# Kernel optimization log

Hardware: AMD Instinct MI355X
Metric: run time of the kernel (lower is better)

## Reference

```python
import jax, jax.numpy as jnp
import numpy as np

R = 8  # number_of_remaining_feature_maps
NEG_SLOPE = 0.01  # torch LeakyReLU default


def setup_inputs() -> dict:
    key = jax.random.key(0)
    k0, k1, k2, k3, k4 = jax.random.split(key, 5)
    b, c, D, H, W = 8, 64, 48, 48, 48
    x = jax.random.normal(k0, (b, c, D, H, W), dtype=jnp.float32)
    s = 1.0 / np.sqrt(c)
    w1 = jax.random.uniform(k1, (c, c), jnp.float32, -s, s)
    b1 = jax.random.uniform(k2, (c,), jnp.float32, -s, s)
    w2 = jax.random.uniform(k3, (c, c), jnp.float32, -s, s)
    b2 = jax.random.uniform(k4, (c,), jnp.float32, -s, s)
    return {"x": x, "w1": w1, "b1": b1, "w2": w2, "b2": b2}


def reference(x, w1, b1, w2, b2):
    # x: (b, c, D, H, W)
    y = jnp.mean(x, axis=(2, 3, 4))                       # adaptive avg pool -> (b, c)
    y = jax.nn.leaky_relu(y @ w1.T + b1, NEG_SLOPE)       # Linear + LeakyReLU
    y = jax.nn.sigmoid(y @ w2.T + b2)                     # Linear + Sigmoid
    _, idx = jax.lax.top_k(y, R)                          # (b, R) channel indices
    # batched channel gather: (b, R, D, H, W)
    return jnp.take_along_axis(x, idx[:, :, None, None, None], axis=1)
```

## Files before the change

### kernel.cpp

```cpp
#include <hip/hip_runtime.h>
#include <math.h>

#define NCH 64
#define NB 8
#define RSEL 8
#define SPATIAL 110592
#define S4 27648
#define PARTS 4
#define CHUNK4 (S4 / PARTS)
#define ITERS (CHUNK4 / 256)

__global__ __launch_bounds__(256) void mean_kernel(const float* __restrict__ x,
                                                   float* __restrict__ partials) {
    const int bc   = blockIdx.x >> 2;
    const int part = blockIdx.x & 3;
    const float4* p = (const float4*)(x + (size_t)bc * SPATIAL) + part * CHUNK4;
    float s = 0.f;
    #pragma unroll
    for (int i = 0; i < ITERS; ++i) {
        float4 v = p[i * 256 + threadIdx.x];
        s += (v.x + v.y) + (v.z + v.w);
    }
    #pragma unroll
    for (int o = 32; o >= 1; o >>= 1) s += __shfl_down(s, o, 64);
    __shared__ float ws[4];
    const int lane = threadIdx.x & 63;
    const int wv   = threadIdx.x >> 6;
    if (lane == 0) ws[wv] = s;
    __syncthreads();
    if (threadIdx.x == 0) {
        partials[blockIdx.x] = (ws[0] + ws[1]) + (ws[2] + ws[3]);
    }
}

__global__ __launch_bounds__(64) void mlp_topk_kernel(const float* __restrict__ partials,
                                                      const float* __restrict__ w1,
                                                      const float* __restrict__ b1,
                                                      const float* __restrict__ w2,
                                                      const float* __restrict__ b2,
                                                      int* __restrict__ idx_out) {
    const int j = threadIdx.x;
    __shared__ float m[NB][NCH];
    __shared__ float h[NB][NCH];
    __shared__ float y[NB][NCH];

    #pragma unroll
    for (int b = 0; b < NB; ++b) {
        const float* pp = partials + (size_t)(b * NCH + j) * PARTS;
        m[b][j] = ((pp[0] + pp[1]) + (pp[2] + pp[3])) * (1.0f / (float)SPATIAL);
    }
    __syncthreads();

    float wrow[NCH];
    #pragma unroll 8
    for (int k = 0; k < NCH; ++k) wrow[k] = w1[j * NCH + k];
    float bj = b1[j];
    #pragma unroll
    for (int b = 0; b < NB; ++b) {
        float acc = bj;
        #pragma unroll 8
        for (int k = 0; k < NCH; ++k) acc += m[b][k] * wrow[k];
        h[b][j] = acc > 0.f ? acc : 0.01f * acc;
    }
    __syncthreads();

    #pragma unroll 8
    for (int k = 0; k < NCH; ++k) wrow[k] = w2[j * NCH + k];
    bj = b2[j];
    #pragma unroll
    for (int b = 0; b < NB; ++b) {
        float acc = bj;
        #pragma unroll 8
        for (int k = 0; k < NCH; ++k) acc += h[b][k] * wrow[k];
        y[b][j] = 1.0f / (1.0f + expf(-acc));
    }
    __syncthreads();

    for (int b = 0; b < NB; ++b) {
        float mine = y[b][j];
        #pragma unroll
        for (int r = 0; r < RSEL; ++r) {
            float v = mine;
            int   c = j;
            #pragma unroll
            for (int o = 32; o >= 1; o >>= 1) {
                float ov = __shfl_xor(v, o, 64);
                int   oc = __shfl_xor(c, o, 64);
                if (ov > v || (ov == v && oc < c)) { v = ov; c = oc; }
            }
            if (j == 0) idx_out[b * RSEL + r] = c;
            if (j == c) mine = -INFINITY;
        }
    }
}

__global__ __launch_bounds__(256) void gather_kernel(const float* __restrict__ x,
                                                     const int* __restrict__ idx,
                                                     float* __restrict__ out) {
    const int pair = blockIdx.y;
    const int b    = pair >> 3;
    const int ch   = idx[pair];
    const float4* src = (const float4*)(x + (size_t)(b * NCH + ch) * SPATIAL);
    float4*       dst = (float4*)(out + (size_t)pair * SPATIAL);
    const int base = blockIdx.x * 1024 + threadIdx.x;
    #pragma unroll
    for (int i = 0; i < 4; ++i) {
        dst[base + i * 256] = src[base + i * 256];
    }
}

extern "C" void kernel_launch(void* const* d_in, const int* in_sizes, int n_in,
                              void* d_out, int out_size, void* d_ws, size_t ws_size,
                              hipStream_t stream) {
    const float* x  = (const float*)d_in[0];
    const float* w1 = (const float*)d_in[1];
    const float* b1 = (const float*)d_in[2];
    const float* w2 = (const float*)d_in[3];
    const float* b2 = (const float*)d_in[4];
    float* out = (float*)d_out;

    float* partials = (float*)d_ws;
    int*   idx      = (int*)((char*)d_ws + NB * NCH * PARTS * sizeof(float));

    mean_kernel<<<dim3(NB * NCH * PARTS), dim3(256), 0, stream>>>(x, partials);
    mlp_topk_kernel<<<dim3(1), dim3(64), 0, stream>>>(partials, w1, b1, w2, b2, idx);
    gather_kernel<<<dim3(S4 / 1024, NB * RSEL), dim3(256), 0, stream>>>(x, idx, out);
}
```

Before: 376.5 us.

## Fuse mean reduction with MLP/top-k via last-block atomic counter; nontemporal gather stores

Merges the mean-pool kernel and the single-block MLP/top-k kernel into one launch. Each block bumps an atomic counter and the last block to finish runs the MLP and top-k, which removes one kernel launch and its gap. This adds a memset launch to reset the counter. It also restructures the MLP loops to accumulate all batches per weight load, and the gather kernel now uses nontemporal stores to bypass cache retention.

```diff
diff --git a/kernel.cpp b/kernel.cpp
--- a/kernel.cpp
+++ b/kernel.cpp
@@ -9,87 +9,102 @@
 #define PARTS 4
 #define CHUNK4 (S4 / PARTS)
 #define ITERS (CHUNK4 / 256)
+#define NBLOCKS (NB * NCH * PARTS)
 
-__global__ __launch_bounds__(256) void mean_kernel(const float* __restrict__ x,
-                                                   float* __restrict__ partials) {
+typedef float f4 __attribute__((ext_vector_type(4)));
+
+__global__ __launch_bounds__(256, 8) void mean_mlp_kernel(
+    const float* __restrict__ x,
+    const float* __restrict__ w1, const float* __restrict__ b1,
+    const float* __restrict__ w2, const float* __restrict__ b2,
+    float* __restrict__ partials, int* __restrict__ idx_out,
+    unsigned int* __restrict__ counter)
+{
     const int bc   = blockIdx.x >> 2;
     const int part = blockIdx.x & 3;
-    const float4* p = (const float4*)(x + (size_t)bc * SPATIAL) + part * CHUNK4;
+    const f4* p = (const f4*)(x + (size_t)bc * SPATIAL) + part * CHUNK4;
     float s = 0.f;
     #pragma unroll
     for (int i = 0; i < ITERS; ++i) {
-        float4 v = p[i * 256 + threadIdx.x];
+        f4 v = p[i * 256 + threadIdx.x];
         s += (v.x + v.y) + (v.z + v.w);
     }
     #pragma unroll
     for (int o = 32; o >= 1; o >>= 1) s += __shfl_down(s, o, 64);
-    __shared__ float ws[4];
+    __shared__ float ws4[4];
+    __shared__ int last_flag;
     const int lane = threadIdx.x & 63;
     const int wv   = threadIdx.x >> 6;
-    if (lane == 0) ws[wv] = s;
+    if (lane == 0) ws4[wv] = s;
     __syncthreads();
     if (threadIdx.x == 0) {
-        partials[blockIdx.x] = (ws[0] + ws[1]) + (ws[2] + ws[3]);
+        partials[blockIdx.x] = (ws4[0] + ws4[1]) + (ws4[2] + ws4[3]);
+        __threadfence();
+        unsigned int old = atomicAdd(counter, 1u);
+        last_flag = (old == NBLOCKS - 1) ? 1 : 0;
     }
-}
+    __syncthreads();
+    if (!last_flag) return;
+    __threadfence();
 
-__global__ __launch_bounds__(64) void mlp_topk_kernel(const float* __restrict__ partials,
-                                                      const float* __restrict__ w1,
-                                                      const float* __restrict__ b1,
-                                                      const float* __restrict__ w2,
-                                                      const float* __restrict__ b2,
-                                                      int* __restrict__ idx_out) {
     const int j = threadIdx.x;
     __shared__ float m[NB][NCH];
     __shared__ float h[NB][NCH];
-    __shared__ float y[NB][NCH];
+    __shared__ float yv[NB][NCH];
 
-    #pragma unroll
-    for (int b = 0; b < NB; ++b) {
-        const float* pp = partials + (size_t)(b * NCH + j) * PARTS;
-        m[b][j] = ((pp[0] + pp[1]) + (pp[2] + pp[3])) * (1.0f / (float)SPATIAL);
+    if (j < NCH) {
+        #pragma unroll
+        for (int b = 0; b < NB; ++b) {
+            const float* pp = partials + (size_t)(b * NCH + j) * PARTS;
+            m[b][j] = ((pp[0] + pp[1]) + (pp[2] + pp[3])) * (1.0f / (float)SPATIAL);
+        }
     }
     __syncthreads();
 
-    float wrow[NCH];
-    #pragma unroll 8
-    for (int k = 0; k < NCH; ++k) wrow[k] = w1[j * NCH + k];
-    float bj = b1[j];
-    #pragma unroll
-    for (int b = 0; b < NB; ++b) {
-        float acc = bj;
-        #pragma unroll 8
-        for (int k = 0; k < NCH; ++k) acc += m[b][k] * wrow[k];
-        h[b][j] = acc > 0.f ? acc : 0.01f * acc;
+    if (j < NCH) {
+        float acc[NB];
+        #pragma unroll
+        for (int b = 0; b < NB; ++b) acc[b] = b1[j];
+        for (int k = 0; k < NCH; ++k) {
+            float wk = w1[j * NCH + k];
+            #pragma unroll
+            for (int b = 0; b < NB; ++b) acc[b] += m[b][k] * wk;
+        }
+        #pragma unroll
+        for (int b = 0; b < NB; ++b) h[b][j] = acc[b] > 0.f ? acc[b] : 0.01f * acc[b];
     }
     __syncthreads();
 
-    #pragma unroll 8
-    for (int k = 0; k < NCH; ++k) wrow[k] = w2[j * NCH + k];
-    bj = b2[j];
-    #pragma unroll
-    for (int b = 0; b < NB; ++b) {
-        float acc = bj;
-        #pragma unroll 8
-        for (int k = 0; k < NCH; ++k) acc += h[b][k] * wrow[k];
-        y[b][j] = 1.0f / (1.0f + expf(-acc));
+    if (j < NCH) {
+        float acc[NB];
+        #pragma unroll
+        for (int b = 0; b < NB; ++b) acc[b] = b2[j];
+        for (int k = 0; k < NCH; ++k) {
+            float wk = w2[j * NCH + k];
+            #pragma unroll
+            for (int b = 0; b < NB; ++b) acc[b] += h[b][k] * wk;
+        }
+        #pragma unroll
+        for (int b = 0; b < NB; ++b) yv[b][j] = 1.0f / (1.0f + expf(-acc[b]));
     }
     __syncthreads();
 
-    for (int b = 0; b < NB; ++b) {
-        float mine = y[b][j];
-        #pragma unroll
-        for (int r = 0; r < RSEL; ++r) {
-            float v = mine;
-            int   c = j;
+    if (j < NCH) {
+        for (int b = 0; b < NB; ++b) {
+            float mine = yv[b][j];
             #pragma unroll
-            for (int o = 32; o >= 1; o >>= 1) {
-                float ov = __shfl_xor(v, o, 64);
-                int   oc = __shfl_xor(c, o, 64);
-                if (ov > v || (ov == v && oc < c)) { v = ov; c = oc; }
+            for (int r = 0; r < RSEL; ++r) {
+                float v = mine;
+                int   c = j;
+                #pragma unroll
+                for (int o = 32; o >= 1; o >>= 1) {
+                    float ov = __shfl_xor(v, o, 64);
+                    int   oc = __shfl_xor(c, o, 64);
+                    if (ov > v || (ov == v && oc < c)) { v = ov; c = oc; }
+                }
+                if (j == 0) idx_out[b * RSEL + r] = c;
+                if (j == c) mine = -INFINITY;
             }
-            if (j == 0) idx_out[b * RSEL + r] = c;
-            if (j == c) mine = -INFINITY;
         }
     }
 }
@@ -100,12 +115,13 @@
     const int pair = blockIdx.y;
     const int b    = pair >> 3;
     const int ch   = idx[pair];
-    const float4* src = (const float4*)(x + (size_t)(b * NCH + ch) * SPATIAL);
-    float4*       dst = (float4*)(out + (size_t)pair * SPATIAL);
+    const f4* src = (const f4*)(x + (size_t)(b * NCH + ch) * SPATIAL);
+    f4*       dst = (f4*)(out + (size_t)pair * SPATIAL);
     const int base = blockIdx.x * 1024 + threadIdx.x;
     #pragma unroll
     for (int i = 0; i < 4; ++i) {
-        dst[base + i * 256] = src[base + i * 256];
+        f4 v = src[base + i * 256];
+        __builtin_nontemporal_store(v, &dst[base + i * 256]);
     }
 }
 
@@ -119,10 +135,12 @@
     const float* b2 = (const float*)d_in[4];
     float* out = (float*)d_out;
 
-    float* partials = (float*)d_ws;
-    int*   idx      = (int*)((char*)d_ws + NB * NCH * PARTS * sizeof(float));
+    float*        partials = (float*)d_ws;
+    int*          idx      = (int*)((char*)d_ws + 8192);
+    unsigned int* counter  = (unsigned int*)((char*)d_ws + 8448);
 
-    mean_kernel<<<dim3(NB * NCH * PARTS), dim3(256), 0, stream>>>(x, partials);
-    mlp_topk_kernel<<<dim3(1), dim3(64), 0, stream>>>(partials, w1, b1, w2, b2, idx);
+    hipMemsetAsync(counter, 0, sizeof(unsigned int), stream);
+    mean_mlp_kernel<<<dim3(NBLOCKS), dim3(256), 0, stream>>>(
+        x, w1, b1, w2, b2, partials, idx, counter);
     gather_kernel<<<dim3(S4 / 1024, NB * RSEL), dim3(256), 0, stream>>>(x, idx, out);
 }
```

Result: slower. 464.4 us (+23.3%).
